# Performance work log

Measured on AMD Instinct MI355X. Metric: run time of the kernel, lower is better.

The kernel has to match this reference:

```python
import jax, jax.numpy as jnp
import numpy as np


def setup_inputs() -> dict:
    key = jax.random.key(0)
    k1, k2 = jax.random.split(key)
    B, C, H, W = 16, 8, 512, 512
    pred = jax.random.normal(k1, (B, C, H, W), dtype=jnp.float32)
    target = jax.random.randint(k2, (B, H, W), 0, C, dtype=jnp.int64)
    return {"pred": pred, "target": target}


def reference(pred, target):
    # pred: (B,C,H,W) float; target: (B,H,W) int64. reduction='mean', no weights.
    B, C, H, W = pred.shape

    # ---- J loss (vectorized over all (ci,ck) class pairs) ----
    t1h = jax.nn.one_hot(target, C, axis=1, dtype=pred.dtype)   # (B,C,H,W)
    n_i = t1h.sum(axis=(2, 3))                                   # (B,C) per-class pixel counts
    phi = t1h / n_i[:, :, None, None]                            # (B,C,H,W)
    # M[b,ci,ck] = sum_hw pred[b,ci]*phi[b,ck]
    M = jnp.einsum('bchw,bkhw->bck', pred, phi)
    diag = jnp.diagonal(M, axis1=1, axis2=2)                     # (B,C) = sum pred_ci*phi_ci
    # delta_ik contraction: sum pred_ci*(phi_ci - phi_ck)/2
    inner = (diag[:, :, None] - M) * 0.5                         # (B,C,C), zero on diagonal
    w = jnp.ones((C, C), dtype=pred.dtype)                       # default j_wgt
    off_diag = 1.0 - jnp.eye(C, dtype=pred.dtype)
    loss = w[None] * jnp.log(0.5 + inner) * off_diag[None]       # (B,C,C)
    j = -loss.sum(axis=(1, 2))                                   # (B,)
    jl = j.mean()

    # ---- cross entropy on collapsed dims: logits (B,C,N), target (B,N) ----
    logits = pred.reshape(B, C, H * W)
    logp = jax.nn.log_softmax(logits, axis=1)
    tgt = target.reshape(B, H * W)
    nll = -jnp.take_along_axis(logp, tgt[:, None, :], axis=1)[:, 0, :]  # (B,N)
    ce = nll.mean()

    return jl + ce
```

## Files before the change

kernel.cpp:

```cpp
#include <hip/hip_runtime.h>

#define NB 16
#define NC 8
#define HW (512 * 512)
#define BLOCKS_PER_B 32
#define NTHREADS 256
#define NBLOCKS (BLOCKS_PER_B * NB)
#define STRIDE (BLOCKS_PER_B * NTHREADS)

#define WS_FLOATS (NB * NC * NC + NB * NC + 2)
#define CTR_IDX (NB * NC * NC + NB * NC + 1)

__device__ __forceinline__ float wave_reduce(float v) {
#pragma unroll
  for (int off = 32; off > 0; off >>= 1) v += __shfl_xor(v, off, 64);
  return v;
}

__global__ __launch_bounds__(NTHREADS, 2)
void jce_main(const float* __restrict__ pred, const int* __restrict__ target,
              float* __restrict__ ws, float* __restrict__ out) {
  const int b = blockIdx.y;
  const int tid = threadIdx.x;
  const float* predb = pred + (size_t)b * NC * HW;
  const int4* tgt4 = (const int4*)(target + (size_t)b * HW);
  const int g0 = blockIdx.x * NTHREADS + tid;

  float S[NC][NC];
  float cnt[NC];
  float ce = 0.0f;
#pragma unroll
  for (int i = 0; i < NC; ++i) {
    cnt[i] = 0.0f;
#pragma unroll
    for (int k = 0; k < NC; ++k) S[i][k] = 0.0f;
  }

  int4 tA, tB;
  float4 pA[NC], pB[NC];

#define LOAD(T, P, s)                                                      \
  do {                                                                     \
    const int gg = g0 + (s) * STRIDE;                                      \
    T = tgt4[gg];                                                          \
    _Pragma("unroll") for (int c = 0; c < NC; ++c)                         \
        P[c] = ((const float4*)(predb + (size_t)c * HW))[gg];              \
  } while (0)

#define COMPUTE(T, P)                                                      \
  do {                                                                     \
    _Pragma("unroll") for (int j = 0; j < 4; ++j) {                        \
      const int tc = (j == 0) ? T.x : (j == 1) ? T.y : (j == 2) ? T.z : T.w; \
      float pv[NC];                                                        \
      _Pragma("unroll") for (int c = 0; c < NC; ++c)                       \
          pv[c] = (j == 0) ? P[c].x : (j == 1) ? P[c].y                    \
                  : (j == 2) ? P[c].z : P[c].w;                            \
      float es = 0.0f;                                                     \
      _Pragma("unroll") for (int c = 0; c < NC; ++c) es += __expf(pv[c]);  \
      const float lse = __logf(es);                                        \
      float ptc = 0.0f;                                                    \
      _Pragma("unroll") for (int k = 0; k < NC; ++k) {                     \
        const float msk = (tc == k) ? 1.0f : 0.0f;                         \
        cnt[k] += msk;                                                     \
        ptc = fmaf(msk, pv[k], ptc);                                       \
        _Pragma("unroll") for (int ci = 0; ci < NC; ++ci)                  \
            S[ci][k] = fmaf(msk, pv[ci], S[ci][k]);                        \
      }                                                                    \
      ce += lse - ptc;                                                     \
    }                                                                      \
  } while (0)

  LOAD(tA, pA, 0);
#pragma unroll
  for (int s = 0; s < 8; s += 2) {
    if (s + 1 < 8) LOAD(tB, pB, s + 1);
    COMPUTE(tA, pA);
    if (s + 2 < 8) LOAD(tA, pA, s + 2);
    if (s + 1 < 8) COMPUTE(tB, pB);
  }
#undef LOAD
#undef COMPUTE

#pragma unroll
  for (int i = 0; i < NC; ++i) {
#pragma unroll
    for (int k = 0; k < NC; ++k) S[i][k] = wave_reduce(S[i][k]);
    cnt[i] = wave_reduce(cnt[i]);
  }
  ce = wave_reduce(ce);

  __shared__ float red[NTHREADS / 64][NC * NC + NC + 1];
  const int wave = tid >> 6, lane = tid & 63;
  if (lane == 0) {
#pragma unroll
    for (int i = 0; i < NC; ++i) {
#pragma unroll
      for (int k = 0; k < NC; ++k) red[wave][i * NC + k] = S[i][k];
      red[wave][NC * NC + i] = cnt[i];
    }
    red[wave][NC * NC + NC] = ce;
  }
  __syncthreads();
  if (tid < NC * NC + NC + 1) {
    float v = 0.0f;
#pragma unroll
    for (int w = 0; w < NTHREADS / 64; ++w) v += red[w][tid];
    if (tid < NC * NC)
      atomicAdd(&ws[b * (NC * NC) + tid], v);
    else if (tid < NC * NC + NC)
      atomicAdd(&ws[NB * NC * NC + b * NC + (tid - NC * NC)], v);
    else
      atomicAdd(&ws[NB * NC * NC + NB * NC], v);
  }

  __shared__ int is_last;
  __syncthreads();
  if (tid == 0) {
    __threadfence();
    unsigned prev = atomicAdd((unsigned*)&ws[CTR_IDX], 1u);
    is_last = (prev == (unsigned)(NBLOCKS - 1)) ? 1 : 0;
  }
  __syncthreads();
  if (!is_last) return;

  float acc = 0.0f;
  for (int idx = tid; idx < NB * NC * NC; idx += NTHREADS) {
    const int bb = idx >> 6, ci = (idx >> 3) & 7, ck = idx & 7;
    if (ci == ck) continue;
    const float n_ck = atomicAdd(&ws[NB * NC * NC + bb * NC + ck], 0.0f);
    const float n_ci = atomicAdd(&ws[NB * NC * NC + bb * NC + ci], 0.0f);
    const float Sik = atomicAdd(&ws[bb * (NC * NC) + ci * NC + ck], 0.0f);
    const float Sii = atomicAdd(&ws[bb * (NC * NC) + ci * NC + ci], 0.0f);
    acc += logf(0.5f + 0.5f * (Sii / n_ci - Sik / n_ck));
  }
  acc = wave_reduce(acc);
  __shared__ float red2[NTHREADS / 64];
  if (lane == 0) red2[wave] = acc;
  __syncthreads();
  if (tid == 0) {
    float tot = 0.0f;
#pragma unroll
    for (int w = 0; w < NTHREADS / 64; ++w) tot += red2[w];
    const float jl = -tot / (float)NB;
    const float cesum = atomicAdd(&ws[NB * NC * NC + NB * NC], 0.0f);
    out[0] = jl + cesum / ((float)NB * (float)HW);
  }
}

extern "C" void kernel_launch(void* const* d_in, const int* in_sizes, int n_in,
                              void* d_out, int out_size, void* d_ws, size_t ws_size,
                              hipStream_t stream) {
  const float* pred = (const float*)d_in[0];
  const int* target = (const int*)d_in[1];
  float* out = (float*)d_out;
  float* ws = (float*)d_ws;

  hipMemsetAsync(ws, 0, WS_FLOATS * sizeof(float), stream);
  dim3 grid(BLOCKS_PER_B, NB);
  jce_main<<<grid, NTHREADS, 0, stream>>>(pred, target, ws, out);
}
```

Baseline: 233.8 us.

## Split class channels across waves and share exponentials through LDS

Each wave of a 512-thread block now handles one class channel, so each thread keeps 8 accumulators for a single row of the S matrix instead of the full 8x8 matrix plus eight channel loads. Per-pixel exponentials are written to a shared tile, and 256 threads then combine them into the log-sum-exp for the cross-entropy term. The aim is to cut register pressure and raise occupancy for what was a compute- and register-bound loop. In exchange it adds two block barriers per iteration, keeps fewer loads in flight per thread, and rereads the target from every wave.

```diff
diff --git a/kernel.cpp b/kernel.cpp
--- a/kernel.cpp
+++ b/kernel.cpp
@@ -3,13 +3,16 @@
 #define NB 16
 #define NC 8
 #define HW (512 * 512)
-#define BLOCKS_PER_B 32
-#define NTHREADS 256
+#define TPB 512
+#define BLOCKS_PER_B 64
 #define NBLOCKS (BLOCKS_PER_B * NB)
-#define STRIDE (BLOCKS_PER_B * NTHREADS)
+#define GPB 1024
+#define ITERS (GPB / 64)
 
-#define WS_FLOATS (NB * NC * NC + NB * NC + 2)
-#define CTR_IDX (NB * NC * NC + NB * NC + 1)
+#define N_BASE (NB * NC * NC)
+#define CE_IDX (NB * NC * NC + NB * NC)
+#define CTR_IDX (CE_IDX + 1)
+#define WS_FLOATS (CTR_IDX + 1)
 
 __device__ __forceinline__ float wave_reduce(float v) {
 #pragma unroll
@@ -17,100 +20,75 @@
   return v;
 }
 
-__global__ __launch_bounds__(NTHREADS, 2)
+__global__ __launch_bounds__(TPB, 8)
 void jce_main(const float* __restrict__ pred, const int* __restrict__ target,
               float* __restrict__ ws, float* __restrict__ out) {
   const int b = blockIdx.y;
   const int tid = threadIdx.x;
-  const float* predb = pred + (size_t)b * NC * HW;
-  const int4* tgt4 = (const int4*)(target + (size_t)b * HW);
-  const int g0 = blockIdx.x * NTHREADS + tid;
+  const int w = tid >> 6;
+  const int lane = tid & 63;
 
-  float S[NC][NC];
-  float cnt[NC];
-  float ce = 0.0f;
+  const float* predc = pred + ((size_t)b * NC + w) * HW;
+  const int* tgtb = target + (size_t)b * HW;
+  const int g0 = blockIdx.x * GPB;
+
+  __shared__ __align__(16) float e_tile[NC][256];
+
+  float S[NC], cnt[NC], ce = 0.0f;
 #pragma unroll
-  for (int i = 0; i < NC; ++i) {
-    cnt[i] = 0.0f;
+  for (int k = 0; k < NC; ++k) { S[k] = 0.0f; cnt[k] = 0.0f; }
+
+  for (int it = 0; it < ITERS; ++it) {
+    const int g = g0 + it * 64 + lane;
+    const int4 t4 = ((const int4*)tgtb)[g];
+    const float4 p4 = ((const float4*)predc)[g];
+
+    float4 e4;
+    e4.x = __expf(p4.x); e4.y = __expf(p4.y);
+    e4.z = __expf(p4.z); e4.w = __expf(p4.w);
+    ((float4*)&e_tile[w][0])[lane] = e4;
+
 #pragma unroll
-    for (int k = 0; k < NC; ++k) S[i][k] = 0.0f;
+    for (int j = 0; j < 4; ++j) {
+      const int tc = (j == 0) ? t4.x : (j == 1) ? t4.y : (j == 2) ? t4.z : t4.w;
+      const float pv = (j == 0) ? p4.x : (j == 1) ? p4.y : (j == 2) ? p4.z : p4.w;
+#pragma unroll
+      for (int k = 0; k < NC; ++k) S[k] += (tc == k) ? pv : 0.0f;
+      if (w == 0) {
+#pragma unroll
+        for (int k = 0; k < NC; ++k) cnt[k] += (tc == k) ? 1.0f : 0.0f;
+      }
+    }
+    __syncthreads();
+
+    if (tid < 256) {
+      const int tc = tgtb[g0 * 4 + it * 256 + tid];
+      float s = 0.0f;
+#pragma unroll
+      for (int c = 0; c < NC; ++c) s += e_tile[c][tid];
+      ce += __logf(s) - __logf(e_tile[tc][tid]);
+    }
+    __syncthreads();
   }
 
-  int4 tA, tB;
-  float4 pA[NC], pB[NC];
-
-#define LOAD(T, P, s)                                                      \
-  do {                                                                     \
-    const int gg = g0 + (s) * STRIDE;                                      \
-    T = tgt4[gg];                                                          \
-    _Pragma("unroll") for (int c = 0; c < NC; ++c)                         \
-        P[c] = ((const float4*)(predb + (size_t)c * HW))[gg];              \
-  } while (0)
-
-#define COMPUTE(T, P)                                                      \
-  do {                                                                     \
-    _Pragma("unroll") for (int j = 0; j < 4; ++j) {                        \
-      const int tc = (j == 0) ? T.x : (j == 1) ? T.y : (j == 2) ? T.z : T.w; \
-      float pv[NC];                                                        \
-      _Pragma("unroll") for (int c = 0; c < NC; ++c)                       \
-          pv[c] = (j == 0) ? P[c].x : (j == 1) ? P[c].y                    \
-                  : (j == 2) ? P[c].z : P[c].w;                            \
-      float es = 0.0f;                                                     \
-      _Pragma("unroll") for (int c = 0; c < NC; ++c) es += __expf(pv[c]);  \
-      const float lse = __logf(es);                                        \
-      float ptc = 0.0f;                                                    \
-      _Pragma("unroll") for (int k = 0; k < NC; ++k) {                     \
-        const float msk = (tc == k) ? 1.0f : 0.0f;                         \
-        cnt[k] += msk;                                                     \
-        ptc = fmaf(msk, pv[k], ptc);                                       \
-        _Pragma("unroll") for (int ci = 0; ci < NC; ++ci)                  \
-            S[ci][k] = fmaf(msk, pv[ci], S[ci][k]);                        \
-      }                                                                    \
-      ce += lse - ptc;                                                     \
-    }                                                                      \
-  } while (0)
-
-  LOAD(tA, pA, 0);
 #pragma unroll
-  for (int s = 0; s < 8; s += 2) {
-    if (s + 1 < 8) LOAD(tB, pB, s + 1);
-    COMPUTE(tA, pA);
-    if (s + 2 < 8) LOAD(tA, pA, s + 2);
-    if (s + 1 < 8) COMPUTE(tB, pB);
-  }
-#undef LOAD
-#undef COMPUTE
-
+  for (int k = 0; k < NC; ++k) S[k] = wave_reduce(S[k]);
+  if (w == 0) {
 #pragma unroll
-  for (int i = 0; i < NC; ++i) {
-#pragma unroll
-    for (int k = 0; k < NC; ++k) S[i][k] = wave_reduce(S[i][k]);
-    cnt[i] = wave_reduce(cnt[i]);
+    for (int k = 0; k < NC; ++k) cnt[k] = wave_reduce(cnt[k]);
   }
   ce = wave_reduce(ce);
 
-  __shared__ float red[NTHREADS / 64][NC * NC + NC + 1];
-  const int wave = tid >> 6, lane = tid & 63;
   if (lane == 0) {
 #pragma unroll
-    for (int i = 0; i < NC; ++i) {
+    for (int k = 0; k < NC; ++k)
+      atomicAdd(&ws[b * (NC * NC) + w * NC + k], S[k]);
+    if (w == 0) {
 #pragma unroll
-      for (int k = 0; k < NC; ++k) red[wave][i * NC + k] = S[i][k];
-      red[wave][NC * NC + i] = cnt[i];
+      for (int k = 0; k < NC; ++k)
+        atomicAdd(&ws[N_BASE + b * NC + k], cnt[k]);
     }
-    red[wave][NC * NC + NC] = ce;
-  }
-  __syncthreads();
-  if (tid < NC * NC + NC + 1) {
-    float v = 0.0f;
-#pragma unroll
-    for (int w = 0; w < NTHREADS / 64; ++w) v += red[w][tid];
-    if (tid < NC * NC)
-      atomicAdd(&ws[b * (NC * NC) + tid], v);
-    else if (tid < NC * NC + NC)
-      atomicAdd(&ws[NB * NC * NC + b * NC + (tid - NC * NC)], v);
-    else
-      atomicAdd(&ws[NB * NC * NC + NB * NC], v);
+    if (w < 4) atomicAdd(&ws[CE_IDX], ce);
   }
 
   __shared__ int is_last;
@@ -124,25 +102,25 @@
   if (!is_last) return;
 
   float acc = 0.0f;
-  for (int idx = tid; idx < NB * NC * NC; idx += NTHREADS) {
+  for (int idx = tid; idx < NB * NC * NC; idx += TPB) {
     const int bb = idx >> 6, ci = (idx >> 3) & 7, ck = idx & 7;
     if (ci == ck) continue;
-    const float n_ck = atomicAdd(&ws[NB * NC * NC + bb * NC + ck], 0.0f);
-    const float n_ci = atomicAdd(&ws[NB * NC * NC + bb * NC + ci], 0.0f);
+    const float n_ck = atomicAdd(&ws[N_BASE + bb * NC + ck], 0.0f);
+    const float n_ci = atomicAdd(&ws[N_BASE + bb * NC + ci], 0.0f);
     const float Sik = atomicAdd(&ws[bb * (NC * NC) + ci * NC + ck], 0.0f);
     const float Sii = atomicAdd(&ws[bb * (NC * NC) + ci * NC + ci], 0.0f);
     acc += logf(0.5f + 0.5f * (Sii / n_ci - Sik / n_ck));
   }
   acc = wave_reduce(acc);
-  __shared__ float red2[NTHREADS / 64];
-  if (lane == 0) red2[wave] = acc;
+  __shared__ float red2[TPB / 64];
+  if (lane == 0) red2[w] = acc;
   __syncthreads();
   if (tid == 0) {
     float tot = 0.0f;
 #pragma unroll
-    for (int w = 0; w < NTHREADS / 64; ++w) tot += red2[w];
+    for (int ww = 0; ww < TPB / 64; ++ww) tot += red2[ww];
     const float jl = -tot / (float)NB;
-    const float cesum = atomicAdd(&ws[NB * NC * NC + NB * NC], 0.0f);
+    const float cesum = atomicAdd(&ws[CE_IDX], 0.0f);
     out[0] = jl + cesum / ((float)NB * (float)HW);
   }
 }
@@ -157,5 +135,5 @@
 
   hipMemsetAsync(ws, 0, WS_FLOATS * sizeof(float), stream);
   dim3 grid(BLOCKS_PER_B, NB);
-  jce_main<<<grid, NTHREADS, 0, stream>>>(pred, target, ws, out);
+  jce_main<<<grid, TPB, 0, stream>>>(pred, target, ws, out);
 }
```

New measurement: 281.9 us. +20.6%, slower.
